# Optimization experiments

Measured on AMD Instinct MI355X. Metric: run time of the kernel, lower is better.

The kernel has to match this reference:

```python
import jax, jax.numpy as jnp
import numpy as np

EMBED_DIMS = 1024
NUM_HEADS = 16
HEAD_DIMS = EMBED_DIMS // NUM_HEADS


def setup_inputs() -> dict:
    key = jax.random.key(0)
    k_x, k_wqkv, k_bqkv, k_wp, k_bp = jax.random.split(key, 5)
    B, N, D = 2, 2048, EMBED_DIMS
    x = jax.random.normal(k_x, (B, N, D), dtype=jnp.float32)
    # torch nn.Linear(in, out): weight [out, in], y = x @ W.T + b
    s = 1.0 / np.sqrt(D)
    W_qkv = jax.random.uniform(k_wqkv, (3 * D, D), jnp.float32, -s, s)
    b_qkv = jax.random.uniform(k_bqkv, (3 * D,), jnp.float32, -s, s)
    W_proj = jax.random.uniform(k_wp, (D, D), jnp.float32, -s, s)
    b_proj = jax.random.uniform(k_bp, (D,), jnp.float32, -s, s)
    return {"x": x, "W_qkv": W_qkv, "b_qkv": b_qkv, "W_proj": W_proj, "b_proj": b_proj}


def reference(x, W_qkv, b_qkv, W_proj, b_proj):
    B, N, D = x.shape
    H, Hd = NUM_HEADS, HEAD_DIMS
    # qkv projection: [B, N, 3, H, Hd] -> split q, k, v as [B, H, N, Hd]
    qkv = (x @ W_qkv.T + b_qkv).reshape(B, N, 3, H, Hd).transpose(2, 0, 3, 1, 4)
    q, k, v = qkv[0], qkv[1], qkv[2]
    scale = 1.0 / jnp.sqrt(jnp.asarray(Hd, x.dtype))
    attn = jnp.einsum("bhqd,bhkd->bhqk", q, k) * scale  # [B, H, N, N]
    attn = jax.nn.softmax(attn, axis=-1)
    out = jnp.einsum("bhqk,bhkd->bhqd", attn, v)  # [B, H, N, Hd]
    out = out.transpose(0, 2, 1, 3).reshape(B, N, D)
    out = out @ W_proj.T + b_proj
    return out
```

## Files before the change

kernel.cpp:

```cpp
#include <hip/hip_runtime.h>

typedef __attribute__((ext_vector_type(8))) short bf16x8;
typedef __attribute__((ext_vector_type(4))) float f32x4;

static __device__ __forceinline__ unsigned int cvt_pk_bf16(float lo, float hi) {
  unsigned int r;
  asm("v_cvt_pk_bf16_f32 %0, %1, %2" : "=v"(r) : "v"(lo), "v"(hi));
  return r;
}

#define GLOAD_LDS16(gp, lp)                                          \
  __builtin_amdgcn_global_load_lds(                                  \
      (const __attribute__((address_space(1))) unsigned int*)(gp),   \
      (__attribute__((address_space(3))) unsigned int*)(lp), 16, 0, 0)

__global__ __launch_bounds__(256) void cvt_all(
    const float* __restrict__ X, const float* __restrict__ Wq,
    const float* __restrict__ Wp, unsigned short* __restrict__ Xb,
    unsigned short* __restrict__ Wqb, unsigned short* __restrict__ Wpb) {
  const int i = blockIdx.x * 256 + threadIdx.x;
  const float4* src;
  unsigned short* dst;
  int off;
  if (i < 1048576) {
    src = (const float4*)X; dst = Xb; off = i;
  } else if (i < 1835008) {
    src = (const float4*)Wq; dst = Wqb; off = i - 1048576;
  } else {
    src = (const float4*)Wp; dst = Wpb; off = i - 1835008;
  }
  const float4 v = src[off];
  uint2 w;
  w.x = cvt_pk_bf16(v.x, v.y);
  w.y = cvt_pk_bf16(v.z, v.w);
  *(uint2*)(dst + (size_t)off * 4) = w;
}

__global__ __launch_bounds__(256) void qkv_gemm(
    const unsigned short* __restrict__ Xb, const unsigned short* __restrict__ Wb,
    const float* __restrict__ bias, unsigned short* __restrict__ Qb,
    unsigned short* __restrict__ Kb, unsigned short* __restrict__ Vt) {
  __shared__ __align__(16) unsigned short A_sh[128 * 32];
  __shared__ __align__(16) unsigned short B_sh[128 * 32];
  const int n0 = blockIdx.x * 128, m0 = blockIdx.y * 128;
  const int tid = threadIdx.x, lane = tid & 63, wave = tid >> 6;
  const int wr = wave >> 1, wc = wave & 1, lm = lane & 15, lg = lane >> 4;
  const int lrow = lane >> 2, lcol = (lane & 3) * 8;

  f32x4 acc[4][4] = {};

  for (int k0 = 0; k0 < 1024; k0 += 32) {
#pragma unroll
    for (int j = 0; j < 2; ++j) {
      const int chunk = wave * 2 + j;
      const int row = chunk * 16 + lrow;
      GLOAD_LDS16(Xb + (size_t)(m0 + row) * 1024 + k0 + lcol, &A_sh[chunk * 512]);
      GLOAD_LDS16(Wb + (size_t)(n0 + row) * 1024 + k0 + lcol, &B_sh[chunk * 512]);
    }
    __syncthreads();
    bf16x8 af[4], bfr[4];
#pragma unroll
    for (int mi = 0; mi < 4; ++mi)
      af[mi] = *(const bf16x8*)&A_sh[(wr * 64 + mi * 16 + lm) * 32 + lg * 8];
#pragma unroll
    for (int ni = 0; ni < 4; ++ni)
      bfr[ni] = *(const bf16x8*)&B_sh[(wc * 64 + ni * 16 + lm) * 32 + lg * 8];
#pragma unroll
    for (int mi = 0; mi < 4; ++mi)
#pragma unroll
      for (int ni = 0; ni < 4; ++ni)
        acc[mi][ni] = __builtin_amdgcn_mfma_f32_16x16x32_bf16(
            af[mi], bfr[ni], acc[mi][ni], 0, 0, 0);
    __syncthreads();
  }

  const float qscale = 0.18033688011112042f;
#pragma unroll
  for (int mi = 0; mi < 4; ++mi) {
#pragma unroll
    for (int ni = 0; ni < 4; ++ni) {
      const int gn = n0 + wc * 64 + ni * 16 + lm;
      const float bv = bias[gn];
      const int which = gn >> 10;
      const int h = (gn >> 6) & 15;
      const int hd = gn & 63;
      float v[4];
#pragma unroll
      for (int r = 0; r < 4; ++r) v[r] = acc[mi][ni][r] + bv;
      const int gm0 = m0 + wr * 64 + mi * 16 + lg * 4;
      const int bb = gm0 >> 11;
      const int nq0 = gm0 & 2047;
      if (which == 0) {
        const unsigned int p01 = cvt_pk_bf16(v[0] * qscale, v[1] * qscale);
        const unsigned int p23 = cvt_pk_bf16(v[2] * qscale, v[3] * qscale);
        unsigned short* p = Qb + (((size_t)bb * 16 + h) * 2048 + nq0) * 64 + hd;
        p[0] = (unsigned short)p01;  p[64] = (unsigned short)(p01 >> 16);
        p[128] = (unsigned short)p23; p[192] = (unsigned short)(p23 >> 16);
      } else if (which == 1) {
        const unsigned int p01 = cvt_pk_bf16(v[0], v[1]);
        const unsigned int p23 = cvt_pk_bf16(v[2], v[3]);
        unsigned short* p = Kb + (((size_t)bb * 16 + h) * 2048 + nq0) * 64 + hd;
        p[0] = (unsigned short)p01;  p[64] = (unsigned short)(p01 >> 16);
        p[128] = (unsigned short)p23; p[192] = (unsigned short)(p23 >> 16);
      } else {
        uint2 w;
        w.x = cvt_pk_bf16(v[0], v[1]);
        w.y = cvt_pk_bf16(v[2], v[3]);
        *(uint2*)(Vt + (((size_t)bb * 16 + h) * 64 + hd) * 2048 + nq0) = w;
      }
    }
  }
}

__global__ __launch_bounds__(256) void attn_kernel(
    const unsigned short* __restrict__ Qb, const unsigned short* __restrict__ Kb,
    const unsigned short* __restrict__ Vt, unsigned short* __restrict__ Ob) {
  __shared__ __align__(16) unsigned short K_sh[2][2][64 * 32];
  __shared__ __align__(16) unsigned short V_sh[2][2][64 * 32];
  __shared__ __align__(16) unsigned short P_sh[128 * 68];
  const int bh = blockIdx.y, q0 = blockIdx.x * 128;
  const size_t base = (size_t)bh * (2048 * 64);
  const unsigned short* Qp = Qb + base;
  const unsigned short* Kp = Kb + base;
  const unsigned short* Vp = Vt + base;
  const int tid = threadIdx.x, lane = tid & 63, wave = tid >> 6;
  const int lm = lane & 15, lg = lane >> 4;
  const int r4 = lane >> 2;
  const int c8 = (lane & 3) * 8;

  bf16x8 qf[2][2];
#pragma unroll
  for (int mi = 0; mi < 2; ++mi)
#pragma unroll
    for (int kc = 0; kc < 2; ++kc)
      qf[mi][kc] = *(const bf16x8*)(Qp +
          (size_t)(q0 + wave * 32 + mi * 16 + lm) * 64 + kc * 32 + lg * 8);

  f32x4 o[2][4] = {};
  float lsum[2][4] = {};

  const int plane = wave & 1;
  const bool isV = wave >= 2;

#define STAGE(kt_, b_)                                                        \
  do {                                                                        \
    if (!isV) {                                                               \
      _Pragma("unroll")                                                       \
      for (int qv = 0; qv < 4; ++qv)                                          \
        GLOAD_LDS16(Kp + (size_t)((kt_) * 64 + qv * 16 + r4) * 64 +           \
                        plane * 32 + c8,                                      \
                    &K_sh[b_][plane][qv * 512]);                              \
    } else {                                                                  \
      _Pragma("unroll")                                                       \
      for (int qv = 0; qv < 4; ++qv)                                          \
        GLOAD_LDS16(Vp + (size_t)(qv * 16 + r4) * 2048 + (kt_) * 64 +         \
                        plane * 32 + c8,                                      \
                    &V_sh[b_][plane][qv * 512]);                              \
    }                                                                         \
  } while (0)

  STAGE(0, 0);

  for (int kt = 0; kt < 32; ++kt) {
    const int cur = kt & 1;
    __syncthreads();
    if (kt < 31) STAGE(kt + 1, cur ^ 1);

    f32x4 s[2][4] = {};
#pragma unroll
    for (int kc = 0; kc < 2; ++kc) {
#pragma unroll
      for (int ni = 0; ni < 4; ++ni) {
        const bf16x8 kf =
            *(const bf16x8*)&K_sh[cur][kc][(ni * 16 + lm) * 32 + lg * 8];
#pragma unroll
        for (int mi = 0; mi < 2; ++mi)
          s[mi][ni] = __builtin_amdgcn_mfma_f32_16x16x32_bf16(
              qf[mi][kc], kf, s[mi][ni], 0, 0, 0);
      }
    }

#pragma unroll
    for (int mi = 0; mi < 2; ++mi)
#pragma unroll
      for (int ni = 0; ni < 4; ++ni) {
        float p0 = exp2f(s[mi][ni][0]), p1 = exp2f(s[mi][ni][1]);
        float p2 = exp2f(s[mi][ni][2]), p3 = exp2f(s[mi][ni][3]);
        lsum[mi][0] += p0; lsum[mi][1] += p1;
        lsum[mi][2] += p2; lsum[mi][3] += p3;
        const unsigned int a = cvt_pk_bf16(p0, p1);
        const unsigned int b = cvt_pk_bf16(p2, p3);
        unsigned short* pp =
            &P_sh[(wave * 32 + mi * 16 + lg * 4) * 68 + ni * 16 + lm];
        pp[0] = (unsigned short)a;    pp[68] = (unsigned short)(a >> 16);
        pp[136] = (unsigned short)b;  pp[204] = (unsigned short)(b >> 16);
      }

#pragma unroll
    for (int kc = 0; kc < 2; ++kc) {
      bf16x8 pa[2];
#pragma unroll
      for (int mi = 0; mi < 2; ++mi)
        pa[mi] = *(const bf16x8*)&P_sh[(wave * 32 + mi * 16 + lm) * 68 +
                                       kc * 32 + lg * 8];
#pragma unroll
      for (int ni = 0; ni < 4; ++ni) {
        const bf16x8 vb =
            *(const bf16x8*)&V_sh[cur][kc][(ni * 16 + lm) * 32 + lg * 8];
#pragma unroll
        for (int mi = 0; mi < 2; ++mi)
          o[mi][ni] = __builtin_amdgcn_mfma_f32_16x16x32_bf16(
              pa[mi], vb, o[mi][ni], 0, 0, 0);
      }
    }
  }
#undef STAGE

  const int b = bh >> 4, h = bh & 15;
#pragma unroll
  for (int mi = 0; mi < 2; ++mi)
#pragma unroll
    for (int r = 0; r < 4; ++r) {
      float l = lsum[mi][r];
      l += __shfl_xor(l, 1);
      l += __shfl_xor(l, 2);
      l += __shfl_xor(l, 4);
      l += __shfl_xor(l, 8);
      const float inv = 1.0f / l;
      const int nq = q0 + wave * 32 + mi * 16 + lg * 4 + r;
      unsigned short* p = Ob + ((size_t)(b * 2048 + nq) * 16 + h) * 64 + lm;
      const unsigned int a = cvt_pk_bf16(o[mi][0][r] * inv, o[mi][1][r] * inv);
      const unsigned int c = cvt_pk_bf16(o[mi][2][r] * inv, o[mi][3][r] * inv);
      p[0] = (unsigned short)a;   p[16] = (unsigned short)(a >> 16);
      p[32] = (unsigned short)c;  p[48] = (unsigned short)(c >> 16);
    }
}

__global__ __launch_bounds__(256) void proj_gemm(
    const unsigned short* __restrict__ A, const unsigned short* __restrict__ Wb,
    const float* __restrict__ bias, float* __restrict__ Out) {
  __shared__ __align__(16) unsigned short A_sh[64 * 32];
  __shared__ __align__(16) unsigned short B_sh[128 * 32];
  const int n0 = blockIdx.x * 128, m0 = blockIdx.y * 64;
  const int tid = threadIdx.x, lane = tid & 63, wave = tid >> 6;
  const int wr = wave >> 1, wc = wave & 1, lm = lane & 15, lg = lane >> 4;
  const int lrow = lane >> 2, lcol = (lane & 3) * 8;

  f32x4 acc[2][4] = {};

  for (int k0 = 0; k0 < 1024; k0 += 32) {
    {
      const int row = wave * 16 + lrow;
      GLOAD_LDS16(A + (size_t)(m0 + row) * 1024 + k0 + lcol, &A_sh[wave * 512]);
    }
#pragma unroll
    for (int j = 0; j < 2; ++j) {
      const int chunk = wave * 2 + j;
      const int row = chunk * 16 + lrow;
      GLOAD_LDS16(Wb + (size_t)(n0 + row) * 1024 + k0 + lcol, &B_sh[chunk * 512]);
    }
    __syncthreads();
    bf16x8 af[2], bfr[4];
#pragma unroll
    for (int mi = 0; mi < 2; ++mi)
      af[mi] = *(const bf16x8*)&A_sh[(wr * 32 + mi * 16 + lm) * 32 + lg * 8];
#pragma unroll
    for (int ni = 0; ni < 4; ++ni)
      bfr[ni] = *(const bf16x8*)&B_sh[(wc * 64 + ni * 16 + lm) * 32 + lg * 8];
#pragma unroll
    for (int mi = 0; mi < 2; ++mi)
#pragma unroll
      for (int ni = 0; ni < 4; ++ni)
        acc[mi][ni] = __builtin_amdgcn_mfma_f32_16x16x32_bf16(
            af[mi], bfr[ni], acc[mi][ni], 0, 0, 0);
    __syncthreads();
  }

#pragma unroll
  for (int mi = 0; mi < 2; ++mi)
#pragma unroll
    for (int ni = 0; ni < 4; ++ni) {
      const int gn = n0 + wc * 64 + ni * 16 + lm;
      const float bv = bias[gn];
#pragma unroll
      for (int r = 0; r < 4; ++r) {
        const int gm = m0 + wr * 32 + mi * 16 + lg * 4 + r;
        Out[(size_t)gm * 1024 + gn] = acc[mi][ni][r] + bv;
      }
    }
}

extern "C" void kernel_launch(void* const* d_in, const int* in_sizes, int n_in,
                              void* d_out, int out_size, void* d_ws, size_t ws_size,
                              hipStream_t stream) {
  const float* x      = (const float*)d_in[0];
  const float* W_qkv  = (const float*)d_in[1];
  const float* b_qkv  = (const float*)d_in[2];
  const float* W_proj = (const float*)d_in[3];
  const float* b_proj = (const float*)d_in[4];
  float* out = (float*)d_out;

  unsigned short* Qb  = (unsigned short*)d_ws;
  unsigned short* Kb  = Qb + 4194304;
  unsigned short* Vt  = Kb + 4194304;
  unsigned short* Ao  = Vt + 4194304;
  unsigned short* Xb  = Ao + 4194304;
  unsigned short* Wqb = Xb + 4194304;
  unsigned short* Wpb = Wqb + 3145728;

  cvt_all<<<8192, 256, 0, stream>>>(x, W_qkv, W_proj, Xb, Wqb, Wpb);
  qkv_gemm<<<dim3(24, 32), 256, 0, stream>>>(Xb, Wqb, b_qkv, Qb, Kb, Vt);
  attn_kernel<<<dim3(16, 32), 256, 0, stream>>>(Qb, Kb, Vt, Ao);
  proj_gemm<<<dim3(8, 64), 256, 0, stream>>>(Ao, Wpb, b_proj, out);
}
```

Measured before the change: 211.0 us.

## Switch pipeline from bf16 to fp16 MFMA and swizzle K/V LDS tiles

Converts all intermediate tensors and MFMA ops from bf16 to fp16 across every kernel, replacing packed bf16 conversions with per-element half casts. It also XOR-swizzles the K and V shared-memory layout in the attention kernel to reduce LDS bank conflicts, and uses the hardware exp2 builtin. The fp16 range is narrower, so unnormalized softmax exponentials or large activations could overflow, and per-element conversions may cost more instructions than packed ones.

```diff
diff --git a/kernel.cpp b/kernel.cpp
--- a/kernel.cpp
+++ b/kernel.cpp
@@ -1,13 +1,17 @@
 #include <hip/hip_runtime.h>
 
-typedef __attribute__((ext_vector_type(8))) short bf16x8;
+typedef _Float16 f16x8 __attribute__((ext_vector_type(8)));
 typedef __attribute__((ext_vector_type(4))) float f32x4;
 
-static __device__ __forceinline__ unsigned int cvt_pk_bf16(float lo, float hi) {
-  unsigned int r;
-  asm("v_cvt_pk_bf16_f32 %0, %1, %2" : "=v"(r) : "v"(lo), "v"(hi));
-  return r;
-}
+static __device__ __forceinline__ unsigned short f2h(float f) {
+  return __builtin_bit_cast(unsigned short, (_Float16)f);
+}
+
+#if __has_builtin(__builtin_amdgcn_exp2f)
+#define EXP2(x) __builtin_amdgcn_exp2f(x)
+#else
+#define EXP2(x) exp2f(x)
+#endif
 
 #define GLOAD_LDS16(gp, lp)                                          \
   __builtin_amdgcn_global_load_lds(                                  \
@@ -30,10 +34,8 @@
     src = (const float4*)Wp; dst = Wpb; off = i - 1835008;
   }
   const float4 v = src[off];
-  uint2 w;
-  w.x = cvt_pk_bf16(v.x, v.y);
-  w.y = cvt_pk_bf16(v.z, v.w);
-  *(uint2*)(dst + (size_t)off * 4) = w;
+  *(ushort4*)(dst + (size_t)off * 4) =
+      make_ushort4(f2h(v.x), f2h(v.y), f2h(v.z), f2h(v.w));
 }
 
 __global__ __launch_bounds__(256) void qkv_gemm(
@@ -58,18 +60,18 @@
       GLOAD_LDS16(Wb + (size_t)(n0 + row) * 1024 + k0 + lcol, &B_sh[chunk * 512]);
     }
     __syncthreads();
-    bf16x8 af[4], bfr[4];
+    f16x8 af[4], bfr[4];
 #pragma unroll
     for (int mi = 0; mi < 4; ++mi)
-      af[mi] = *(const bf16x8*)&A_sh[(wr * 64 + mi * 16 + lm) * 32 + lg * 8];
+      af[mi] = *(const f16x8*)&A_sh[(wr * 64 + mi * 16 + lm) * 32 + lg * 8];
 #pragma unroll
     for (int ni = 0; ni < 4; ++ni)
-      bfr[ni] = *(const bf16x8*)&B_sh[(wc * 64 + ni * 16 + lm) * 32 + lg * 8];
+      bfr[ni] = *(const f16x8*)&B_sh[(wc * 64 + ni * 16 + lm) * 32 + lg * 8];
 #pragma unroll
     for (int mi = 0; mi < 4; ++mi)
 #pragma unroll
       for (int ni = 0; ni < 4; ++ni)
-        acc[mi][ni] = __builtin_amdgcn_mfma_f32_16x16x32_bf16(
+        acc[mi][ni] = __builtin_amdgcn_mfma_f32_16x16x32_f16(
             af[mi], bfr[ni], acc[mi][ni], 0, 0, 0);
     __syncthreads();
   }
@@ -91,22 +93,16 @@
       const int bb = gm0 >> 11;
       const int nq0 = gm0 & 2047;
       if (which == 0) {
-        const unsigned int p01 = cvt_pk_bf16(v[0] * qscale, v[1] * qscale);
-        const unsigned int p23 = cvt_pk_bf16(v[2] * qscale, v[3] * qscale);
         unsigned short* p = Qb + (((size_t)bb * 16 + h) * 2048 + nq0) * 64 + hd;
-        p[0] = (unsigned short)p01;  p[64] = (unsigned short)(p01 >> 16);
-        p[128] = (unsigned short)p23; p[192] = (unsigned short)(p23 >> 16);
+        p[0] = f2h(v[0] * qscale);   p[64] = f2h(v[1] * qscale);
+        p[128] = f2h(v[2] * qscale); p[192] = f2h(v[3] * qscale);
       } else if (which == 1) {
-        const unsigned int p01 = cvt_pk_bf16(v[0], v[1]);
-        const unsigned int p23 = cvt_pk_bf16(v[2], v[3]);
         unsigned short* p = Kb + (((size_t)bb * 16 + h) * 2048 + nq0) * 64 + hd;
-        p[0] = (unsigned short)p01;  p[64] = (unsigned short)(p01 >> 16);
-        p[128] = (unsigned short)p23; p[192] = (unsigned short)(p23 >> 16);
+        p[0] = f2h(v[0]);   p[64] = f2h(v[1]);
+        p[128] = f2h(v[2]); p[192] = f2h(v[3]);
       } else {
-        uint2 w;
-        w.x = cvt_pk_bf16(v[0], v[1]);
-        w.y = cvt_pk_bf16(v[2], v[3]);
-        *(uint2*)(Vt + (((size_t)bb * 16 + h) * 64 + hd) * 2048 + nq0) = w;
+        *(ushort4*)(Vt + (((size_t)bb * 16 + h) * 64 + hd) * 2048 + nq0) =
+            make_ushort4(f2h(v[0]), f2h(v[1]), f2h(v[2]), f2h(v[3]));
       }
     }
   }
@@ -126,14 +122,15 @@
   const int tid = threadIdx.x, lane = tid & 63, wave = tid >> 6;
   const int lm = lane & 15, lg = lane >> 4;
   const int r4 = lane >> 2;
-  const int c8 = (lane & 3) * 8;
-
-  bf16x8 qf[2][2];
+  const int sg8 = (((lane & 3) ^ ((r4 >> 1) & 3)) * 8);
+  const int lgx = (lg ^ ((lm >> 1) & 3)) * 8;
+
+  f16x8 qf[2][2];
 #pragma unroll
   for (int mi = 0; mi < 2; ++mi)
 #pragma unroll
     for (int kc = 0; kc < 2; ++kc)
-      qf[mi][kc] = *(const bf16x8*)(Qp +
+      qf[mi][kc] = *(const f16x8*)(Qp +
           (size_t)(q0 + wave * 32 + mi * 16 + lm) * 64 + kc * 32 + lg * 8);
 
   f32x4 o[2][4] = {};
@@ -148,13 +145,13 @@
       _Pragma("unroll")                                                       \
       for (int qv = 0; qv < 4; ++qv)                                          \
         GLOAD_LDS16(Kp + (size_t)((kt_) * 64 + qv * 16 + r4) * 64 +           \
-                        plane * 32 + c8,                                      \
+                        plane * 32 + sg8,                                     \
                     &K_sh[b_][plane][qv * 512]);                              \
     } else {                                                                  \
       _Pragma("unroll")                                                       \
       for (int qv = 0; qv < 4; ++qv)                                          \
         GLOAD_LDS16(Vp + (size_t)(qv * 16 + r4) * 2048 + (kt_) * 64 +         \
-                        plane * 32 + c8,                                      \
+                        plane * 32 + sg8,                                     \
                     &V_sh[b_][plane][qv * 512]);                              \
     }                                                                         \
   } while (0)
@@ -171,11 +168,11 @@
     for (int kc = 0; kc < 2; ++kc) {
 #pragma unroll
       for (int ni = 0; ni < 4; ++ni) {
-        const bf16x8 kf =
-            *(const bf16x8*)&K_sh[cur][kc][(ni * 16 + lm) * 32 + lg * 8];
+        const f16x8 kf =
+            *(const f16x8*)&K_sh[cur][kc][(ni * 16 + lm) * 32 + lgx];
 #pragma unroll
         for (int mi = 0; mi < 2; ++mi)
-          s[mi][ni] = __builtin_amdgcn_mfma_f32_16x16x32_bf16(
+          s[mi][ni] = __builtin_amdgcn_mfma_f32_16x16x32_f16(
               qf[mi][kc], kf, s[mi][ni], 0, 0, 0);
       }
     }
@@ -184,32 +181,30 @@
     for (int mi = 0; mi < 2; ++mi)
 #pragma unroll
       for (int ni = 0; ni < 4; ++ni) {
-        float p0 = exp2f(s[mi][ni][0]), p1 = exp2f(s[mi][ni][1]);
-        float p2 = exp2f(s[mi][ni][2]), p3 = exp2f(s[mi][ni][3]);
+        float p0 = EXP2(s[mi][ni][0]), p1 = EXP2(s[mi][ni][1]);
+        float p2 = EXP2(s[mi][ni][2]), p3 = EXP2(s[mi][ni][3]);
         lsum[mi][0] += p0; lsum[mi][1] += p1;
         lsum[mi][2] += p2; lsum[mi][3] += p3;
-        const unsigned int a = cvt_pk_bf16(p0, p1);
-        const unsigned int b = cvt_pk_bf16(p2, p3);
         unsigned short* pp =
             &P_sh[(wave * 32 + mi * 16 + lg * 4) * 68 + ni * 16 + lm];
-        pp[0] = (unsigned short)a;    pp[68] = (unsigned short)(a >> 16);
-        pp[136] = (unsigned short)b;  pp[204] = (unsigned short)(b >> 16);
+        pp[0] = f2h(p0);    pp[68] = f2h(p1);
+        pp[136] = f2h(p2);  pp[204] = f2h(p3);
       }
 
 #pragma unroll
     for (int kc = 0; kc < 2; ++kc) {
-      bf16x8 pa[2];
+      f16x8 pa[2];
 #pragma unroll
       for (int mi = 0; mi < 2; ++mi)
-        pa[mi] = *(const bf16x8*)&P_sh[(wave * 32 + mi * 16 + lm) * 68 +
-                                       kc * 32 + lg * 8];
+        pa[mi] = *(const f16x8*)&P_sh[(wave * 32 + mi * 16 + lm) * 68 +
+                                      kc * 32 + lg * 8];
 #pragma unroll
       for (int ni = 0; ni < 4; ++ni) {
-        const bf16x8 vb =
-            *(const bf16x8*)&V_sh[cur][kc][(ni * 16 + lm) * 32 + lg * 8];
+        const f16x8 vb =
+            *(const f16x8*)&V_sh[cur][kc][(ni * 16 + lm) * 32 + lgx];
 #pragma unroll
         for (int mi = 0; mi < 2; ++mi)
-          o[mi][ni] = __builtin_amdgcn_mfma_f32_16x16x32_bf16(
+          o[mi][ni] = __builtin_amdgcn_mfma_f32_16x16x32_f16(
               pa[mi], vb, o[mi][ni], 0, 0, 0);
       }
     }
@@ -229,10 +224,10 @@
       const float inv = 1.0f / l;
       const int nq = q0 + wave * 32 + mi * 16 + lg * 4 + r;
       unsigned short* p = Ob + ((size_t)(b * 2048 + nq) * 16 + h) * 64 + lm;
-      const unsigned int a = cvt_pk_bf16(o[mi][0][r] * inv, o[mi][1][r] * inv);
-      const unsigned int c = cvt_pk_bf16(o[mi][2][r] * inv, o[mi][3][r] * inv);
-      p[0] = (unsigned short)a;   p[16] = (unsigned short)(a >> 16);
-      p[32] = (unsigned short)c;  p[48] = (unsigned short)(c >> 16);
+      p[0] = f2h(o[mi][0][r] * inv);
+      p[16] = f2h(o[mi][1][r] * inv);
+      p[32] = f2h(o[mi][2][r] * inv);
+      p[48] = f2h(o[mi][3][r] * inv);
     }
 }
 
@@ -260,18 +255,18 @@
       GLOAD_LDS16(Wb + (size_t)(n0 + row) * 1024 + k0 + lcol, &B_sh[chunk * 512]);
     }
     __syncthreads();
-    bf16x8 af[2], bfr[4];
+    f16x8 af[2], bfr[4];
 #pragma unroll
     for (int mi = 0; mi < 2; ++mi)
-      af[mi] = *(const bf16x8*)&A_sh[(wr * 32 + mi * 16 + lm) * 32 + lg * 8];
+      af[mi] = *(const f16x8*)&A_sh[(wr * 32 + mi * 16 + lm) * 32 + lg * 8];
 #pragma unroll
     for (int ni = 0; ni < 4; ++ni)
-      bfr[ni] = *(const bf16x8*)&B_sh[(wc * 64 + ni * 16 + lm) * 32 + lg * 8];
+      bfr[ni] = *(const f16x8*)&B_sh[(wc * 64 + ni * 16 + lm) * 32 + lg * 8];
 #pragma unroll
     for (int mi = 0; mi < 2; ++mi)
 #pragma unroll
       for (int ni = 0; ni < 4; ++ni)
-        acc[mi][ni] = __builtin_amdgcn_mfma_f32_16x16x32_bf16(
+        acc[mi][ni] = __builtin_amdgcn_mfma_f32_16x16x32_f16(
             af[mi], bfr[ni], acc[mi][ni], 0, 0, 0);
     __syncthreads();
   }
```

After: 197.8 us. 1.07x faster.
